# Performance work log

Hardware: AMD Instinct MI355X
Metric: run time of the kernel (lower is better)

## Reference

```python
import jax, jax.numpy as jnp
import numpy as np

B, S, DIM = 1, 2048, 4096
NH, NKV, HD = 32, 8, 128
REPEATS = NH // NKV
ROPE_THETA = 10000.0


def setup_inputs() -> dict:
    key = jax.random.key(0)
    ks = jax.random.split(key, 6)
    x = jax.random.normal(ks[0], (B, S, DIM), jnp.float32) * 0.02
    wq = jax.random.normal(ks[1], (NH * HD, DIM), jnp.float32) * 0.02
    wk = jax.random.normal(ks[2], (NKV * HD, DIM), jnp.float32) * 0.02
    wv = jax.random.normal(ks[3], (NKV * HD, DIM), jnp.float32) * 0.02
    wo = jax.random.normal(ks[4], (DIM, NH * HD), jnp.float32) * 0.02
    # rotary frequencies (real cos/sin form of complex freqs_cis)
    inv_freq = 1.0 / (ROPE_THETA ** (jnp.arange(0, HD, 2, dtype=jnp.float32) / HD))
    ang = jnp.arange(S, dtype=jnp.float32)[:, None] * inv_freq[None, :]  # [S, HD//2]
    freqs_cos = jnp.cos(ang)
    freqs_sin = jnp.sin(ang)
    positions = jnp.arange(S, dtype=jnp.int32)  # prompt phase: all positions
    # additive causal mask
    mask = jnp.where(jnp.tril(jnp.ones((S, S), bool)), 0.0, -1e9).astype(jnp.float32)
    cache_k = jnp.zeros((B, S, NKV, HD), jnp.float32)
    cache_v = jnp.zeros((B, S, NKV, HD), jnp.float32)
    return dict(x=x, wq=wq, wk=wk, wv=wv, wo=wo, freqs_cos=freqs_cos,
                freqs_sin=freqs_sin, cache_k=cache_k, cache_v=cache_v,
                positions=positions, mask=mask)


def apply_rope(t, cos, sin):
    # t: [b, s, h, d]; pairs are (d0,d1),(d2,d3),... matching view_as_complex
    tr = t[..., 0::2]
    ti = t[..., 1::2]
    c = cos[None, :, None, :]
    s = sin[None, :, None, :]
    out_r = tr * c - ti * s
    out_i = tr * s + ti * c
    return jnp.stack([out_r, out_i], axis=-1).reshape(t.shape)


def reference(x, wq, wk, wv, wo, freqs_cos, freqs_sin, cache_k, cache_v, positions, mask):
    b, s, _ = x.shape
    xq = jnp.einsum('bsd,od->bso', x, wq).reshape(b, s, NH, HD)
    xk = jnp.einsum('bsd,od->bso', x, wk).reshape(b, s, NKV, HD)
    xv = jnp.einsum('bsd,od->bso', x, wv).reshape(b, s, NKV, HD)
    xq = apply_rope(xq, freqs_cos, freqs_sin)
    xk = apply_rope(xk, freqs_cos, freqs_sin)
    # KV-cache scatter (prompt phase writes; output uses fresh xk/xv here)
    cache_k = cache_k.at[:, positions].set(xk)
    cache_v = cache_v.at[:, positions].set(xv)
    # GQA: repeat_interleave kv heads to match query heads
    k = jnp.repeat(xk, REPEATS, axis=2).transpose(0, 2, 1, 3)  # [b, NH, s, HD]
    v = jnp.repeat(xv, REPEATS, axis=2).transpose(0, 2, 1, 3)
    q = xq.transpose(0, 2, 1, 3)
    scale = HD ** -0.5
    scores = jnp.einsum('bhqd,bhkd->bhqk', q, k) * scale + mask[None, None]
    probs = jax.nn.softmax(scores.astype(jnp.float32), axis=-1).astype(q.dtype)
    out = jnp.einsum('bhqk,bhkd->bhqd', probs, v)
    out = out.transpose(0, 2, 1, 3).reshape(b, s, NH * HD)
    return jnp.einsum('bso,do->bsd', out, wo)
```

## Files before the change

### kernel.cpp

```cpp
#include <hip/hip_runtime.h>
#include <hip/hip_bf16.h>
#include <stdint.h>

typedef __bf16 bf16_t;
typedef __attribute__((ext_vector_type(8))) __bf16 bf16x8;
typedef __attribute__((ext_vector_type(4))) float f32x4;
typedef __attribute__((ext_vector_type(8))) unsigned short u16x8;

#define S_LEN 2048
#define DIM   4096
#define QKVN  6144
#define NHEAD 32
#define HDIM  128

typedef __attribute__((address_space(1))) unsigned int as1_u32;
typedef __attribute__((address_space(3))) unsigned int as3_u32;

__device__ __forceinline__ unsigned short f2bf(float f) {
  unsigned u = __builtin_bit_cast(unsigned, f);
  u += 0x7fffu + ((u >> 16) & 1u);
  return (unsigned short)(u >> 16);
}

__device__ __forceinline__ void gload_lds16(const void* g, void* l) {
  __builtin_amdgcn_global_load_lds(
      (as1_u32*)(unsigned long long)(uintptr_t)g,
      (as3_u32*)(unsigned int)(uintptr_t)l,
      16, 0, 0);
}

__global__ __launch_bounds__(256) void cvt5_kernel(const float* __restrict__ x,
                                                   const float* __restrict__ wq,
                                                   const float* __restrict__ wk,
                                                   const float* __restrict__ wv,
                                                   const float* __restrict__ wo,
                                                   ushort4* __restrict__ xb,
                                                   ushort4* __restrict__ wqkvb,
                                                   ushort4* __restrict__ wob) {
  const long N0 = 2097152;
  const long N1 = N0 + 4194304;
  const long N2 = N1 + 1048576;
  const long N3 = N2 + 1048576;
  const long N4 = N3 + 4194304;
  long idx = (long)blockIdx.x * 256 + threadIdx.x;
  long stride = (long)gridDim.x * 256;
  for (long i = idx; i < N4; i += stride) {
    const float4* s; ushort4* d; long o;
    if (i < N0)      { s = (const float4*)x;  d = xb;              o = i; }
    else if (i < N1) { s = (const float4*)wq; d = wqkvb;           o = i - N0; }
    else if (i < N2) { s = (const float4*)wk; d = wqkvb + 4194304; o = i - N1; }
    else if (i < N3) { s = (const float4*)wv; d = wqkvb + 5242880; o = i - N2; }
    else             { s = (const float4*)wo; d = wob;             o = i - N3; }
    float4 v = s[o];
    ushort4 r;
    r.x = f2bf(v.x); r.y = f2bf(v.y); r.z = f2bf(v.z); r.w = f2bf(v.w);
    d[o] = r;
  }
}

__device__ __forceinline__ bf16x8 fld(const char* half, int row, int chunk) {
  return *(const bf16x8*)(half + row * 128 + ((chunk ^ (row & 7)) << 4));
}

template <int OUTF32>
__global__ __launch_bounds__(512, 2) void gemm8q(const bf16_t* __restrict__ A,
                                                 const bf16_t* __restrict__ B,
                                                 void* __restrict__ Cout,
                                                 int M, int N, int K, int nxt) {
  __shared__ char lds[114688];
  const int tid = threadIdx.x;
  const int lane = tid & 63, w = tid >> 6;
  const int wm = w >> 2, wn = w & 3;
  const int lg = lane >> 4, lr = lane & 15;
  const int nwg = gridDim.x;
  const int orig = blockIdx.x;
  const int wgid = (orig & 7) * (nwg >> 3) + (orig >> 3);
  const int bx = wgid % nxt, by = wgid / nxt;
  const long rowA = (long)by * 256;
  const long rowB = (long)bx * 192;

  f32x4 acc[8][3];
  const f32x4 z4 = {0.f, 0.f, 0.f, 0.f};
#pragma unroll
  for (int i = 0; i < 8; ++i)
#pragma unroll
    for (int j = 0; j < 3; ++j) acc[i][j] = z4;

  const int r0 = tid >> 3, sl = tid & 7;
  const long xo  = (long)((sl ^ (r0 & 7)) << 3);
  const long aof = (rowA + r0) * (long)K + xo;
  const long bof = (rowB + r0) * (long)K + xo;
  const long j1  = (long)64 * K;
  const long h1  = (long)128 * K;
  const int ld0 = tid * 16, ld1 = (tid + 512) * 16, ld2 = (tid + 1024) * 16;

#define QSTG_A(K0, HALF, DBUF)                                                 \
  { char* hp = lds + (DBUF) * 57344 + (HALF) * 16384;                          \
    gload_lds16(A + aof + (HALF) * h1 + (K0),      hp + ld0);                  \
    gload_lds16(A + aof + (HALF) * h1 + j1 + (K0), hp + ld1); }
#define QSTG_B(K0, DBUF)                                                       \
  { char* bp = lds + (DBUF) * 57344 + 32768;                                   \
    gload_lds16(B + bof + (K0),          bp + ld0);                            \
    gload_lds16(B + bof + j1 + (K0),     bp + ld1);                            \
    gload_lds16(B + bof + 2 * j1 + (K0), bp + ld2); }

  const int nt = K >> 6;
  const int brow = wn * 48;

  QSTG_A(0, 0, 0); QSTG_A(0, 1, 0); QSTG_B(0, 0);
  QSTG_B(64, 1);
  asm volatile("s_waitcnt vmcnt(3)" ::: "memory");
  __builtin_amdgcn_s_barrier();

  bf16x8 af[8][2], bf_[3][2];

  for (int t = 0; t < nt; ++t) {
    const int d = t & 1;
    const char* Ah = lds + d * 57344 + wm * 16384;
    const char* Br = lds + d * 57344 + 32768;
    const int k1 = (t + 1) << 6, k2 = (t + 2) << 6;
#pragma unroll
    for (int m = 0; m < 2; ++m) {
      af[m][0] = fld(Ah, m * 16 + lr, lg);
      af[m][1] = fld(Ah, m * 16 + lr, 4 + lg);
    }
#pragma unroll
    for (int n = 0; n < 3; ++n) {
      bf_[n][0] = fld(Br, brow + n * 16 + lr, lg);
      bf_[n][1] = fld(Br, brow + n * 16 + lr, 4 + lg);
    }
    if (t + 1 < nt) QSTG_A(k1, 0, d ^ 1);
    __builtin_amdgcn_s_barrier();
    asm volatile("s_waitcnt lgkmcnt(0)" ::: "memory");
    __builtin_amdgcn_sched_barrier(0);
    __builtin_amdgcn_s_setprio(1);
#pragma unroll
    for (int m = 0; m < 2; ++m)
#pragma unroll
      for (int n = 0; n < 3; ++n) {
        acc[m][n] = __builtin_amdgcn_mfma_f32_16x16x32_bf16(af[m][0], bf_[n][0], acc[m][n], 0, 0, 0);
        acc[m][n] = __builtin_amdgcn_mfma_f32_16x16x32_bf16(af[m][1], bf_[n][1], acc[m][n], 0, 0, 0);
      }
    __builtin_amdgcn_s_setprio(0);
    __builtin_amdgcn_s_barrier();
#pragma unroll
    for (int m = 2; m < 4; ++m) {
      af[m][0] = fld(Ah, m * 16 + lr, lg);
      af[m][1] = fld(Ah, m * 16 + lr, 4 + lg);
    }
    if (t + 1 < nt) QSTG_A(k1, 1, d ^ 1);
    __builtin_amdgcn_s_barrier();
    asm volatile("s_waitcnt lgkmcnt(0)" ::: "memory");
    __builtin_amdgcn_sched_barrier(0);
    __builtin_amdgcn_s_setprio(1);
#pragma unroll
    for (int m = 2; m < 4; ++m)
#pragma unroll
      for (int n = 0; n < 3; ++n) {
        acc[m][n] = __builtin_amdgcn_mfma_f32_16x16x32_bf16(af[m][0], bf_[n][0], acc[m][n], 0, 0, 0);
        acc[m][n] = __builtin_amdgcn_mfma_f32_16x16x32_bf16(af[m][1], bf_[n][1], acc[m][n], 0, 0, 0);
      }
    __builtin_amdgcn_s_setprio(0);
    __builtin_amdgcn_s_barrier();
#pragma unroll
    for (int m = 4; m < 6; ++m) {
      af[m][0] = fld(Ah, m * 16 + lr, lg);
      af[m][1] = fld(Ah, m * 16 + lr, 4 + lg);
    }
    if (t + 2 < nt) QSTG_B(k2, d);
    __builtin_amdgcn_s_barrier();
    asm volatile("s_waitcnt lgkmcnt(0)" ::: "memory");
    __builtin_amdgcn_sched_barrier(0);
    __builtin_amdgcn_s_setprio(1);
#pragma unroll
    for (int m = 4; m < 6; ++m)
#pragma unroll
      for (int n = 0; n < 3; ++n) {
        acc[m][n] = __builtin_amdgcn_mfma_f32_16x16x32_bf16(af[m][0], bf_[n][0], acc[m][n], 0, 0, 0);
        acc[m][n] = __builtin_amdgcn_mfma_f32_16x16x32_bf16(af[m][1], bf_[n][1], acc[m][n], 0, 0, 0);
      }
    __builtin_amdgcn_s_setprio(0);
    __builtin_amdgcn_s_barrier();
#pragma unroll
    for (int m = 6; m < 8; ++m) {
      af[m][0] = fld(Ah, m * 16 + lr, lg);
      af[m][1] = fld(Ah, m * 16 + lr, 4 + lg);
    }
    __builtin_amdgcn_s_barrier();
    asm volatile("s_waitcnt lgkmcnt(0)" ::: "memory");
    __builtin_amdgcn_sched_barrier(0);
    __builtin_amdgcn_s_setprio(1);
#pragma unroll
    for (int m = 6; m < 8; ++m)
#pragma unroll
      for (int n = 0; n < 3; ++n) {
        acc[m][n] = __builtin_amdgcn_mfma_f32_16x16x32_bf16(af[m][0], bf_[n][0], acc[m][n], 0, 0, 0);
        acc[m][n] = __builtin_amdgcn_mfma_f32_16x16x32_bf16(af[m][1], bf_[n][1], acc[m][n], 0, 0, 0);
      }
    __builtin_amdgcn_s_setprio(0);
    if (t + 2 < nt) {
      asm volatile("s_waitcnt vmcnt(3)" ::: "memory");
    } else {
      asm volatile("s_waitcnt vmcnt(0)" ::: "memory");
    }
    __builtin_amdgcn_s_barrier();
  }
#undef QSTG_A
#undef QSTG_B

  const long crow = rowA + wm * 128;
  const long ccol = rowB + wn * 48;
  unsigned short* C = (unsigned short*)Cout;
#pragma unroll
  for (int mf = 0; mf < 8; ++mf)
#pragma unroll
    for (int j = 0; j < 4; ++j) {
      long row = crow + mf * 16 + lg * 4 + j;
      unsigned short* cp = C + row * N + ccol + lr;
#pragma unroll
      for (int nf = 0; nf < 3; ++nf) cp[nf * 16] = f2bf(acc[mf][nf][j]);
    }
}

template <int OUTF32>
__global__ __launch_bounds__(512, 2) void gemm2p(const bf16_t* __restrict__ A,
                                                 const bf16_t* __restrict__ B,
                                                 void* __restrict__ Cout,
                                                 int M, int N, int K, int nxt) {
  __shared__ char lds[147456];
  const int tid = threadIdx.x;
  const int lane = tid & 63, w = tid >> 6;
  const int wm = w >> 1, wn = w & 1;
  const int lg = lane >> 4, lr = lane & 15;
  const int nwg = gridDim.x;
  const int orig = blockIdx.x;
  const int wgid = (orig & 7) * (nwg >> 3) + (orig >> 3);
  const int bx = wgid % nxt, by = wgid / nxt;
  const long rowA = (long)by * 256;
  const long rowB = (long)bx * 128;

  f32x4 acc[4][4];
  const f32x4 z4 = {0.f, 0.f, 0.f, 0.f};
#pragma unroll
  for (int i = 0; i < 4; ++i)
#pragma unroll
    for (int j = 0; j < 4; ++j) acc[i][j] = z4;

  const int r0 = tid >> 3, sl = tid & 7;
  const long xo  = (long)((sl ^ (r0 & 7)) << 3);
  const long aof = (rowA + r0) * (long)K + xo;
  const long bof = (rowB + r0) * (long)K + xo;
  const long r64 = (long)64 * K;

#define PSTG_A(K0, BUF)                                                        \
  { char* ap = lds + (BUF) * 32768;                                            \
    gload_lds16(A + aof + (K0),           ap + tid * 16);                      \
    gload_lds16(A + aof + r64 + (K0),     ap + (tid + 512) * 16);              \
    gload_lds16(A + aof + 2 * r64 + (K0), ap + (tid + 1024) * 16);             \
    gload_lds16(A + aof + 3 * r64 + (K0), ap + (tid + 1536) * 16); }
#define PSTG_B(K0, BUF)                                                        \
  { char* bp = lds + 98304 + (BUF) * 16384;                                    \
    gload_lds16(B + bof + (K0),       bp + tid * 16);                          \
    gload_lds16(B + bof + r64 + (K0), bp + (tid + 512) * 16); }

  const int nt = K >> 6;

  PSTG_A(0, 0); PSTG_B(0, 0); PSTG_A(64, 1); PSTG_B(64, 1);
  asm volatile("s_waitcnt vmcnt(6)" ::: "memory");
  __builtin_amdgcn_s_barrier();

  bf16x8 af[4][2], bf_[4][2];

  for (int t = 0; t < nt; ++t) {
    const int b3 = t % 3, s3 = (t + 2) % 3;
    const char* Ab = lds + b3 * 32768;
    const char* Bb = lds + 98304 + b3 * 16384;
    const int arow = wm * 64, brow = wn * 64;
    const int k2 = (t + 2) << 6;
#pragma unroll
    for (int m = 0; m < 4; ++m) {
      af[m][0] = fld(Ab, arow + m * 16 + lr, lg);
      af[m][1] = fld(Ab, arow + m * 16 + lr, 4 + lg);
    }
#pragma unroll
    for (int n = 0; n < 2; ++n) {
      bf_[n][0] = fld(Bb, brow + n * 16 + lr, lg);
      bf_[n][1] = fld(Bb, brow + n * 16 + lr, 4 + lg);
    }
    if (t + 2 < nt) PSTG_A(k2, s3);
    __builtin_amdgcn_s_barrier();
    asm volatile("s_waitcnt lgkmcnt(0)" ::: "memory");
    __builtin_amdgcn_sched_barrier(0);
    __builtin_amdgcn_s_setprio(1);
#pragma unroll
    for (int m = 0; m < 4; ++m)
#pragma unroll
      for (int n = 0; n < 2; ++n) {
        acc[m][n] = __builtin_amdgcn_mfma_f32_16x16x32_bf16(af[m][0], bf_[n][0], acc[m][n], 0, 0, 0);
        acc[m][n] = __builtin_amdgcn_mfma_f32_16x16x32_bf16(af[m][1], bf_[n][1], acc[m][n], 0, 0, 0);
      }
    __builtin_amdgcn_s_setprio(0);
    __builtin_amdgcn_s_barrier();
#pragma unroll
    for (int n = 2; n < 4; ++n) {
      bf_[n][0] = fld(Bb, brow + n * 16 + lr, lg);
      bf_[n][1] = fld(Bb, brow + n * 16 + lr, 4 + lg);
    }
    if (t + 2 < nt) PSTG_B(k2, s3);
    __builtin_amdgcn_s_barrier();
    asm volatile("s_waitcnt lgkmcnt(0)" ::: "memory");
    __builtin_amdgcn_sched_barrier(0);
    __builtin_amdgcn_s_setprio(1);
#pragma unroll
    for (int m = 0; m < 4; ++m)
#pragma unroll
      for (int n = 2; n < 4; ++n) {
        acc[m][n] = __builtin_amdgcn_mfma_f32_16x16x32_bf16(af[m][0], bf_[n][0], acc[m][n], 0, 0, 0);
        acc[m][n] = __builtin_amdgcn_mfma_f32_16x16x32_bf16(af[m][1], bf_[n][1], acc[m][n], 0, 0, 0);
      }
    __builtin_amdgcn_s_setprio(0);
    if (t + 2 < nt) {
      asm volatile("s_waitcnt vmcnt(6)" ::: "memory");
    } else {
      asm volatile("s_waitcnt vmcnt(0)" ::: "memory");
    }
    __builtin_amdgcn_s_barrier();
  }
#undef PSTG_A
#undef PSTG_B

  const long crow = rowA + wm * 64;
  const long ccol = rowB + wn * 64;
  if (OUTF32) {
    float* C = (float*)Cout;
#pragma unroll
    for (int mf = 0; mf < 4; ++mf)
#pragma unroll
      for (int j = 0; j < 4; ++j) {
        long row = crow + mf * 16 + lg * 4 + j;
        float* cp = C + row * N + ccol + lr;
#pragma unroll
        for (int nf = 0; nf < 4; ++nf) cp[nf * 16] = acc[mf][nf][j];
      }
  } else {
    unsigned short* C = (unsigned short*)Cout;
#pragma unroll
    for (int mf = 0; mf < 4; ++mf)
#pragma unroll
      for (int j = 0; j < 4; ++j) {
        long row = crow + mf * 16 + lg * 4 + j;
        unsigned short* cp = C + row * N + ccol + lr;
#pragma unroll
        for (int nf = 0; nf < 4; ++nf) cp[nf * 16] = f2bf(acc[mf][nf][j]);
      }
  }
}

__global__ __launch_bounds__(256) void rope_kernel(unsigned int* __restrict__ qkv32,
                                                   const float* __restrict__ cosb,
                                                   const float* __restrict__ sinb) {
  int t = blockIdx.x * 256 + threadIdx.x;
  int i  = t & 63;
  int sh = t >> 6;
  int hh = sh % 40;
  int s  = sh / 40;
  int col2 = (hh < 32) ? (hh * 64 + i) : (2048 + (hh - 32) * 64 + i);
  unsigned int* p = qkv32 + (long)s * (QKVN / 2) + col2;
  unsigned int v = *p;
  float tr = __builtin_bit_cast(float, (v & 0xffffu) << 16);
  float ti = __builtin_bit_cast(float, v & 0xffff0000u);
  float c  = cosb[s * 64 + i];
  float sn = sinb[s * 64 + i];
  float orr = tr * c - ti * sn;
  float oi  = tr * sn + ti * c;
  *p = (unsigned int)f2bf(orr) | ((unsigned int)f2bf(oi) << 16);
}

__global__ __launch_bounds__(256) void vtrans_kernel(const bf16_t* __restrict__ qkv,
                                                     bf16_t* __restrict__ vT) {
  const int kh = blockIdx.x;
  const int hd = threadIdx.x & 127;
  const int s0 = blockIdx.y * 16 + (threadIdx.x >> 7) * 8;
  u16x8 v;
#pragma unroll
  for (int e = 0; e < 8; ++e)
    v[e] = *(const unsigned short*)(qkv + (long)(s0 + e) * QKVN + 5120 + kh * HDIM + hd);
  *(u16x8*)(vT + ((long)kh * HDIM + hd) * S_LEN + s0) = v;
}

__global__ __launch_bounds__(512) void attn_kernel(const bf16_t* __restrict__ qkv,
                                                   const bf16_t* __restrict__ vT,
                                                   unsigned short* __restrict__ ob) {
  __shared__ bf16_t Kt[64 * 128];
  __shared__ bf16_t Vt[128 * 64];
  __shared__ bf16_t Pl[8 * 16 * 64];
  const int h  = blockIdx.x;
  const int qi = 15 - (int)blockIdx.y;
  const int qb = qi * 128;
  const int kh = h >> 2;
  const int tid = threadIdx.x, lane = tid & 63, w = tid >> 6;
  const int lg = lane >> 4, lr = lane & 15;
  const int qrow0 = qb + w * 16;

  bf16x8 qf[4];
  const bf16_t* qptr = qkv + (long)(qrow0 + lr) * QKVN + h * HDIM + lg * 8;
#pragma unroll
  for (int kk = 0; kk < 4; ++kk) qf[kk] = *(const bf16x8*)(qptr + kk * 32);

  const f32x4 z4 = {0.f, 0.f, 0.f, 0.f};
  f32x4 oacc[8];
#pragma unroll
  for (int c = 0; c < 8; ++c) oacc[c] = z4;
  float m[4]    = {-1e30f, -1e30f, -1e30f, -1e30f};
  float lsum[4] = {0.f, 0.f, 0.f, 0.f};

  char* KtB = (char*)Kt;
  char* VtB = (char*)Vt;
  char* PlB = (char*)Pl + w * 2048;
  const float SCL2 = 0.08838834764831845f * 1.44269504088896f;
  const int ntiles = 2 * qi + 2;
  const int wqmax = qrow0 + 15;

  for (int t = 0; t < ntiles; ++t) {
    const int kv0 = t * 64;
    __syncthreads();
#pragma unroll
    for (int it = 0; it < 2; ++it) {
      int cch = tid + it * 512;
      int r = cch >> 4, c = cch & 15;
      const bf16_t* src = qkv + (long)(kv0 + r) * QKVN + 4096 + kh * HDIM
                          + ((c ^ (r & 7)) * 8);
      gload_lds16(src, KtB + cch * 16);
    }
#pragma unroll
    for (int it = 0; it < 2; ++it) {
      int cch = tid + it * 512;
      int hd = cch >> 3, c = cch & 7;
      const bf16_t* src = vT + ((long)kh * HDIM + hd) * S_LEN + kv0
                          + ((c ^ (hd & 7)) * 8);
      gload_lds16(src, VtB + cch * 16);
    }
    __syncthreads();
    if (kv0 > wqmax) continue;

    f32x4 sf[4];
#pragma unroll
    for (int f = 0; f < 4; ++f) {
      f32x4 a = z4;
      int n = f * 16 + lr;
      int rb = n * 256, sw = (n & 7) << 4;
#pragma unroll
      for (int kk = 0; kk < 4; ++kk) {
        bf16x8 kf = *(const bf16x8*)(KtB + rb + (((kk * 4 + lg) * 16) ^ sw));
        a = __builtin_amdgcn_mfma_f32_16x16x32_bf16(qf[kk], kf, a, 0, 0, 0);
      }
      sf[f] = a;
    }

    float sv[4][4], mx[4];
    if (kv0 + 63 <= qrow0) {
#pragma unroll
      for (int j = 0; j < 4; ++j) {
#pragma unroll
        for (int f = 0; f < 4; ++f) sv[j][f] = sf[f][j] * SCL2;
        float t0 = fmaxf(fmaxf(sv[j][0], sv[j][1]), fmaxf(sv[j][2], sv[j][3]));
        t0 = fmaxf(t0, __shfl_xor(t0, 1));
        t0 = fmaxf(t0, __shfl_xor(t0, 2));
        t0 = fmaxf(t0, __shfl_xor(t0, 4));
        t0 = fmaxf(t0, __shfl_xor(t0, 8));
        mx[j] = t0;
      }
    } else {
#pragma unroll
      for (int j = 0; j < 4; ++j) {
        int qrow = qrow0 + lg * 4 + j;
#pragma unroll
        for (int f = 0; f < 4; ++f) {
          float s = sf[f][j] * SCL2;
          if (kv0 + f * 16 + lr > qrow) s = -1e9f;
          sv[j][f] = s;
        }
        float t0 = fmaxf(fmaxf(sv[j][0], sv[j][1]), fmaxf(sv[j][2], sv[j][3]));
        t0 = fmaxf(t0, __shfl_xor(t0, 1));
        t0 = fmaxf(t0, __shfl_xor(t0, 2));
        t0 = fmaxf(t0, __shfl_xor(t0, 4));
        t0 = fmaxf(t0, __shfl_xor(t0, 8));
        mx[j] = t0;
      }
    }
    float g = fmaxf(fmaxf(mx[0] - m[0], mx[1] - m[1]),
                    fmaxf(mx[2] - m[2], mx[3] - m[3]));
    if (__any(g > 0.f)) {
#pragma unroll
      for (int j = 0; j < 4; ++j) {
        float mn = fmaxf(m[j], mx[j]);
        float sc;
        asm("v_exp_f32 %0, %1" : "=v"(sc) : "v"(m[j] - mn));
        lsum[j] *= sc;
        m[j] = mn;
#pragma unroll
        for (int c = 0; c < 8; ++c) oacc[c][j] *= sc;
      }
    }
#pragma unroll
    for (int j = 0; j < 4; ++j) {
      float p[4];
#pragma unroll
      for (int f = 0; f < 4; ++f)
        asm("v_exp_f32 %0, %1" : "=v"(p[f]) : "v"(sv[j][f] - m[j]));
      float ps = (p[0] + p[1]) + (p[2] + p[3]);
      ps += __shfl_xor(ps, 1);
      ps += __shfl_xor(ps, 2);
      ps += __shfl_xor(ps, 4);
      ps += __shfl_xor(ps, 8);
      lsum[j] += ps;
      int row = lg * 4 + j;
      int swp = (row & 7) << 4;
#pragma unroll
      for (int f = 0; f < 4; ++f)
        *(unsigned short*)(PlB + row * 128 + (((f * 16 + lr) * 2) ^ swp)) = f2bf(p[f]);
    }

    bf16x8 pfr[2];
#pragma unroll
    for (int kk = 0; kk < 2; ++kk)
      pfr[kk] = *(const bf16x8*)(PlB + lr * 128 + (((kk * 4 + lg) * 16) ^ ((lr & 7) << 4)));
#pragma unroll
    for (int c = 0; c < 8; ++c) {
      int hd = c * 16 + lr;
      int rb = hd * 128, sw = (hd & 7) << 4;
#pragma unroll
      for (int kk = 0; kk < 2; ++kk) {
        bf16x8 vf = *(const bf16x8*)(VtB + rb + (((kk * 4 + lg) * 16) ^ sw));
        oacc[c] = __builtin_amdgcn_mfma_f32_16x16x32_bf16(pfr[kk], vf, oacc[c], 0, 0, 0);
      }
    }
  }

  float rl[4];
#pragma unroll
  for (int j = 0; j < 4; ++j) rl[j] = 1.f / lsum[j];
#pragma unroll
  for (int c = 0; c < 8; ++c)
#pragma unroll
    for (int j = 0; j < 4; ++j) {
      long row = qrow0 + lg * 4 + j;
      ob[row * 4096 + h * 128 + c * 16 + lr] = f2bf(oacc[c][j] * rl[j]);
    }
}

extern "C" void kernel_launch(void* const* d_in, const int* in_sizes, int n_in,
                              void* d_out, int out_size, void* d_ws, size_t ws_size,
                              hipStream_t stream) {
  const float* x  = (const float*)d_in[0];
  const float* wq = (const float*)d_in[1];
  const float* wk = (const float*)d_in[2];
  const float* wv = (const float*)d_in[3];
  const float* wo = (const float*)d_in[4];
  const float* fc = (const float*)d_in[5];
  const float* fs = (const float*)d_in[6];

  char* ws = (char*)d_ws;
  bf16_t* xb    = (bf16_t*)(ws + 0);
  bf16_t* wqkvb = (bf16_t*)(ws + 16777216);
  bf16_t* wob   = (bf16_t*)(ws + 67108864);
  bf16_t* qkv   = (bf16_t*)(ws + 100663296);
  bf16_t* ob    = (bf16_t*)(ws + 125829120);
  bf16_t* vT    = (bf16_t*)(ws + 0);

  cvt5_kernel<<<2048, 256, 0, stream>>>(x, wq, wk, wv, wo,
                                        (ushort4*)xb, (ushort4*)wqkvb, (ushort4*)wob);

  gemm8q<0><<<256, 512, 0, stream>>>(xb, wqkvb, qkv, 2048, 6144, 4096, 32);
  vtrans_kernel<<<dim3(8, 128), 256, 0, stream>>>(qkv, vT);
  rope_kernel<<<20480, 256, 0, stream>>>((unsigned int*)qkv, fc, fs);
  attn_kernel<<<dim3(32, 16), 512, 0, stream>>>(qkv, vT, (unsigned short*)ob);
  gemm2p<1><<<256, 512, 0, stream>>>(ob, wob, d_out, 2048, 4096, 4096, 32);
}
```

Before: 320.9 us.

## Deepen GEMM A-tile prefetch to triple buffer and double-buffer attention KV loads

The GEMM kernel now keeps three A-tile stages in LDS (148 KB total) and prefetches A two K-steps ahead, with the vmcnt waits adjusted to match. The attention kernel gets double-buffered K/V LDS tiles, so the loads for tile t+2 are issued while tile t is being computed, replacing the load-then-sync pattern on every iteration. The goal is to hide global-memory latency behind MFMA work. The cost is more LDS per block, which can lower occupancy: the GEMM asks for 2 blocks per CU with 148 KB each, and that may no longer fit.

```diff
diff --git a/kernel.cpp b/kernel.cpp
--- a/kernel.cpp
+++ b/kernel.cpp
@@ -67,7 +67,7 @@
                                                  const bf16_t* __restrict__ B,
                                                  void* __restrict__ Cout,
                                                  int M, int N, int K, int nxt) {
-  __shared__ char lds[114688];
+  __shared__ char lds[147456];
   const int tid = threadIdx.x;
   const int lane = tid & 63, w = tid >> 6;
   const int wm = w >> 2, wn = w & 3;
@@ -94,12 +94,12 @@
   const long h1  = (long)128 * K;
   const int ld0 = tid * 16, ld1 = (tid + 512) * 16, ld2 = (tid + 1024) * 16;
 
-#define QSTG_A(K0, HALF, DBUF)                                                 \
-  { char* hp = lds + (DBUF) * 57344 + (HALF) * 16384;                          \
+#define QSTG_A(K0, HALF, BUF3)                                                 \
+  { char* hp = lds + (BUF3) * 32768 + (HALF) * 16384;                          \
     gload_lds16(A + aof + (HALF) * h1 + (K0),      hp + ld0);                  \
     gload_lds16(A + aof + (HALF) * h1 + j1 + (K0), hp + ld1); }
 #define QSTG_B(K0, DBUF)                                                       \
-  { char* bp = lds + (DBUF) * 57344 + 32768;                                   \
+  { char* bp = lds + 98304 + (DBUF) * 24576;                                   \
     gload_lds16(B + bof + (K0),          bp + ld0);                            \
     gload_lds16(B + bof + j1 + (K0),     bp + ld1);                            \
     gload_lds16(B + bof + 2 * j1 + (K0), bp + ld2); }
@@ -108,17 +108,17 @@
   const int brow = wn * 48;
 
   QSTG_A(0, 0, 0); QSTG_A(0, 1, 0); QSTG_B(0, 0);
-  QSTG_B(64, 1);
-  asm volatile("s_waitcnt vmcnt(3)" ::: "memory");
+  QSTG_A(64, 0, 1); QSTG_A(64, 1, 1); QSTG_B(64, 1);
+  asm volatile("s_waitcnt vmcnt(7)" ::: "memory");
   __builtin_amdgcn_s_barrier();
 
   bf16x8 af[8][2], bf_[3][2];
 
   for (int t = 0; t < nt; ++t) {
-    const int d = t & 1;
-    const char* Ah = lds + d * 57344 + wm * 16384;
-    const char* Br = lds + d * 57344 + 32768;
-    const int k1 = (t + 1) << 6, k2 = (t + 2) << 6;
+    const int a3 = t % 3, s3 = (t + 2) % 3, d = t & 1;
+    const char* Ah = lds + a3 * 32768 + wm * 16384;
+    const char* Br = lds + 98304 + d * 24576;
+    const int k2 = (t + 2) << 6;
 #pragma unroll
     for (int m = 0; m < 2; ++m) {
       af[m][0] = fld(Ah, m * 16 + lr, lg);
@@ -129,7 +129,7 @@
       bf_[n][0] = fld(Br, brow + n * 16 + lr, lg);
       bf_[n][1] = fld(Br, brow + n * 16 + lr, 4 + lg);
     }
-    if (t + 1 < nt) QSTG_A(k1, 0, d ^ 1);
+    if (t + 2 < nt) QSTG_A(k2, 0, s3);
     __builtin_amdgcn_s_barrier();
     asm volatile("s_waitcnt lgkmcnt(0)" ::: "memory");
     __builtin_amdgcn_sched_barrier(0);
@@ -148,7 +148,7 @@
       af[m][0] = fld(Ah, m * 16 + lr, lg);
       af[m][1] = fld(Ah, m * 16 + lr, 4 + lg);
     }
-    if (t + 1 < nt) QSTG_A(k1, 1, d ^ 1);
+    if (t + 2 < nt) QSTG_A(k2, 1, s3);
     __builtin_amdgcn_s_barrier();
     asm volatile("s_waitcnt lgkmcnt(0)" ::: "memory");
     __builtin_amdgcn_sched_barrier(0);
@@ -199,7 +199,7 @@
       }
     __builtin_amdgcn_s_setprio(0);
     if (t + 2 < nt) {
-      asm volatile("s_waitcnt vmcnt(3)" ::: "memory");
+      asm volatile("s_waitcnt vmcnt(7)" ::: "memory");
     } else {
       asm volatile("s_waitcnt vmcnt(0)" ::: "memory");
     }
@@ -391,8 +391,8 @@
 __global__ __launch_bounds__(512) void attn_kernel(const bf16_t* __restrict__ qkv,
                                                    const bf16_t* __restrict__ vT,
                                                    unsigned short* __restrict__ ob) {
-  __shared__ bf16_t Kt[64 * 128];
-  __shared__ bf16_t Vt[128 * 64];
+  __shared__ bf16_t Kt[2][64 * 128];
+  __shared__ bf16_t Vt[2][128 * 64];
   __shared__ bf16_t Pl[8 * 16 * 64];
   const int h  = blockIdx.x;
   const int qi = 15 - (int)blockIdx.y;
@@ -414,128 +414,147 @@
   float m[4]    = {-1e30f, -1e30f, -1e30f, -1e30f};
   float lsum[4] = {0.f, 0.f, 0.f, 0.f};
 
-  char* KtB = (char*)Kt;
-  char* VtB = (char*)Vt;
   char* PlB = (char*)Pl + w * 2048;
   const float SCL2 = 0.08838834764831845f * 1.44269504088896f;
   const int ntiles = 2 * qi + 2;
   const int wqmax = qrow0 + 15;
 
+#define STAGE_KV(T, BUF)                                                       \
+  {                                                                            \
+    const int kvs = (T) * 64;                                                  \
+    _Pragma("unroll")                                                          \
+    for (int it = 0; it < 2; ++it) {                                           \
+      int cch = tid + it * 512;                                                \
+      int r = cch >> 4, c = cch & 15;                                          \
+      gload_lds16(qkv + (long)(kvs + r) * QKVN + 4096 + kh * HDIM              \
+                      + ((c ^ (r & 7)) * 8),                                   \
+                  (char*)Kt[BUF] + cch * 16);                                  \
+    }                                                                          \
+    _Pragma("unroll")                                                          \
+    for (int it = 0; it < 2; ++it) {                                           \
+      int cch = tid + it * 512;                                                \
+      int hd2 = cch >> 3, c = cch & 7;                                         \
+      gload_lds16(vT + ((long)kh * HDIM + hd2) * S_LEN + kvs                   \
+                      + ((c ^ (hd2 & 7)) * 8),                                 \
+                  (char*)Vt[BUF] + cch * 16);                                  \
+    }                                                                          \
+  }
+
+  STAGE_KV(0, 0);
+  STAGE_KV(1, 1);
+  asm volatile("s_waitcnt vmcnt(4)" ::: "memory");
+  __builtin_amdgcn_s_barrier();
+
   for (int t = 0; t < ntiles; ++t) {
     const int kv0 = t * 64;
-    __syncthreads();
-#pragma unroll
-    for (int it = 0; it < 2; ++it) {
-      int cch = tid + it * 512;
-      int r = cch >> 4, c = cch & 15;
-      const bf16_t* src = qkv + (long)(kv0 + r) * QKVN + 4096 + kh * HDIM
-                          + ((c ^ (r & 7)) * 8);
-      gload_lds16(src, KtB + cch * 16);
-    }
-#pragma unroll
-    for (int it = 0; it < 2; ++it) {
-      int cch = tid + it * 512;
-      int hd = cch >> 3, c = cch & 7;
-      const bf16_t* src = vT + ((long)kh * HDIM + hd) * S_LEN + kv0
-                          + ((c ^ (hd & 7)) * 8);
-      gload_lds16(src, VtB + cch * 16);
-    }
-    __syncthreads();
-    if (kv0 > wqmax) continue;
-
-    f32x4 sf[4];
-#pragma unroll
-    for (int f = 0; f < 4; ++f) {
-      f32x4 a = z4;
-      int n = f * 16 + lr;
-      int rb = n * 256, sw = (n & 7) << 4;
-#pragma unroll
-      for (int kk = 0; kk < 4; ++kk) {
-        bf16x8 kf = *(const bf16x8*)(KtB + rb + (((kk * 4 + lg) * 16) ^ sw));
-        a = __builtin_amdgcn_mfma_f32_16x16x32_bf16(qf[kk], kf, a, 0, 0, 0);
-      }
-      sf[f] = a;
-    }
-
-    float sv[4][4], mx[4];
-    if (kv0 + 63 <= qrow0) {
+    const int d = t & 1;
+    if (kv0 <= wqmax) {
+      char* KtB = (char*)Kt[d];
+      char* VtB = (char*)Vt[d];
+
+      f32x4 sf[4];
+#pragma unroll
+      for (int f = 0; f < 4; ++f) {
+        f32x4 a = z4;
+        int n = f * 16 + lr;
+        int rb = n * 256, sw = (n & 7) << 4;
+#pragma unroll
+        for (int kk = 0; kk < 4; ++kk) {
+          bf16x8 kf = *(const bf16x8*)(KtB + rb + (((kk * 4 + lg) * 16) ^ sw));
+          a = __builtin_amdgcn_mfma_f32_16x16x32_bf16(qf[kk], kf, a, 0, 0, 0);
+        }
+        sf[f] = a;
+      }
+
+      float sv[4][4], mx[4];
+      if (kv0 + 63 <= qrow0) {
+#pragma unroll
+        for (int j = 0; j < 4; ++j) {
+#pragma unroll
+          for (int f = 0; f < 4; ++f) sv[j][f] = sf[f][j] * SCL2;
+          float t0 = fmaxf(fmaxf(sv[j][0], sv[j][1]), fmaxf(sv[j][2], sv[j][3]));
+          t0 = fmaxf(t0, __shfl_xor(t0, 1));
+          t0 = fmaxf(t0, __shfl_xor(t0, 2));
+          t0 = fmaxf(t0, __shfl_xor(t0, 4));
+          t0 = fmaxf(t0, __shfl_xor(t0, 8));
+          mx[j] = t0;
+        }
+      } else {
+#pragma unroll
+        for (int j = 0; j < 4; ++j) {
+          int qrow = qrow0 + lg * 4 + j;
+#pragma unroll
+          for (int f = 0; f < 4; ++f) {
+            float s = sf[f][j] * SCL2;
+            if (kv0 + f * 16 + lr > qrow) s = -1e9f;
+            sv[j][f] = s;
+          }
+          float t0 = fmaxf(fmaxf(sv[j][0], sv[j][1]), fmaxf(sv[j][2], sv[j][3]));
+          t0 = fmaxf(t0, __shfl_xor(t0, 1));
+          t0 = fmaxf(t0, __shfl_xor(t0, 2));
+          t0 = fmaxf(t0, __shfl_xor(t0, 4));
+          t0 = fmaxf(t0, __shfl_xor(t0, 8));
+          mx[j] = t0;
+        }
+      }
+      float g = fmaxf(fmaxf(mx[0] - m[0], mx[1] - m[1]),
+                      fmaxf(mx[2] - m[2], mx[3] - m[3]));
+      if (__any(g > 0.f)) {
+#pragma unroll
+        for (int j = 0; j < 4; ++j) {
+          float mn = fmaxf(m[j], mx[j]);
+          float sc;
+          asm("v_exp_f32 %0, %1" : "=v"(sc) : "v"(m[j] - mn));
+          lsum[j] *= sc;
+          m[j] = mn;
+#pragma unroll
+          for (int c = 0; c < 8; ++c) oacc[c][j] *= sc;
+        }
+      }
 #pragma unroll
       for (int j = 0; j < 4; ++j) {
-#pragma unroll
-        for (int f = 0; f < 4; ++f) sv[j][f] = sf[f][j] * SCL2;
-        float t0 = fmaxf(fmaxf(sv[j][0], sv[j][1]), fmaxf(sv[j][2], sv[j][3]));
-        t0 = fmaxf(t0, __shfl_xor(t0, 1));
-        t0 = fmaxf(t0, __shfl_xor(t0, 2));
-        t0 = fmaxf(t0, __shfl_xor(t0, 4));
-        t0 = fmaxf(t0, __shfl_xor(t0, 8));
-        mx[j] = t0;
-      }
+        float p[4];
+#pragma unroll
+        for (int f = 0; f < 4; ++f)
+          asm("v_exp_f32 %0, %1" : "=v"(p[f]) : "v"(sv[j][f] - m[j]));
+        float ps = (p[0] + p[1]) + (p[2] + p[3]);
+        ps += __shfl_xor(ps, 1);
+        ps += __shfl_xor(ps, 2);
+        ps += __shfl_xor(ps, 4);
+        ps += __shfl_xor(ps, 8);
+        lsum[j] += ps;
+        int row = lg * 4 + j;
+        int swp = (row & 7) << 4;
+#pragma unroll
+        for (int f = 0; f < 4; ++f)
+          *(unsigned short*)(PlB + row * 128 + (((f * 16 + lr) * 2) ^ swp)) = f2bf(p[f]);
+      }
+
+      bf16x8 pfr[2];
+#pragma unroll
+      for (int kk = 0; kk < 2; ++kk)
+        pfr[kk] = *(const bf16x8*)(PlB + lr * 128 + (((kk * 4 + lg) * 16) ^ ((lr & 7) << 4)));
+#pragma unroll
+      for (int c = 0; c < 8; ++c) {
+        int hd = c * 16 + lr;
+        int rb = hd * 128, sw = (hd & 7) << 4;
+#pragma unroll
+        for (int kk = 0; kk < 2; ++kk) {
+          bf16x8 vf = *(const bf16x8*)(VtB + rb + (((kk * 4 + lg) * 16) ^ sw));
+          oacc[c] = __builtin_amdgcn_mfma_f32_16x16x32_bf16(pfr[kk], vf, oacc[c], 0, 0, 0);
+        }
+      }
+    }
+    __builtin_amdgcn_s_barrier();
+    if (t + 2 < ntiles) {
+      STAGE_KV(t + 2, d);
+      asm volatile("s_waitcnt vmcnt(4)" ::: "memory");
     } else {
-#pragma unroll
-      for (int j = 0; j < 4; ++j) {
-        int qrow = qrow0 + lg * 4 + j;
-#pragma unroll
-        for (int f = 0; f < 4; ++f) {
-          float s = sf[f][j] * SCL2;
-          if (kv0 + f * 16 + lr > qrow) s = -1e9f;
-          sv[j][f] = s;
-        }
-        float t0 = fmaxf(fmaxf(sv[j][0], sv[j][1]), fmaxf(sv[j][2], sv[j][3]));
-        t0 = fmaxf(t0, __shfl_xor(t0, 1));
-        t0 = fmaxf(t0, __shfl_xor(t0, 2));
-        t0 = fmaxf(t0, __shfl_xor(t0, 4));
-        t0 = fmaxf(t0, __shfl_xor(t0, 8));
-        mx[j] = t0;
-      }
-    }
-    float g = fmaxf(fmaxf(mx[0] - m[0], mx[1] - m[1]),
-                    fmaxf(mx[2] - m[2], mx[3] - m[3]));
-    if (__any(g > 0.f)) {
-#pragma unroll
-      for (int j = 0; j < 4; ++j) {
-        float mn = fmaxf(m[j], mx[j]);
-        float sc;
-        asm("v_exp_f32 %0, %1" : "=v"(sc) : "v"(m[j] - mn));
-        lsum[j] *= sc;
-        m[j] = mn;
-#pragma unroll
-        for (int c = 0; c < 8; ++c) oacc[c][j] *= sc;
-      }
-    }
-#pragma unroll
-    for (int j = 0; j < 4; ++j) {
-      float p[4];
-#pragma unroll
-      for (int f = 0; f < 4; ++f)
-        asm("v_exp_f32 %0, %1" : "=v"(p[f]) : "v"(sv[j][f] - m[j]));
-      float ps = (p[0] + p[1]) + (p[2] + p[3]);
-      ps += __shfl_xor(ps, 1);
-      ps += __shfl_xor(ps, 2);
-      ps += __shfl_xor(ps, 4);
-      ps += __shfl_xor(ps, 8);
-      lsum[j] += ps;
-      int row = lg * 4 + j;
-      int swp = (row & 7) << 4;
-#pragma unroll
-      for (int f = 0; f < 4; ++f)
-        *(unsigned short*)(PlB + row * 128 + (((f * 16 + lr) * 2) ^ swp)) = f2bf(p[f]);
-    }
-
-    bf16x8 pfr[2];
-#pragma unroll
-    for (int kk = 0; kk < 2; ++kk)
-      pfr[kk] = *(const bf16x8*)(PlB + lr * 128 + (((kk * 4 + lg) * 16) ^ ((lr & 7) << 4)));
-#pragma unroll
-    for (int c = 0; c < 8; ++c) {
-      int hd = c * 16 + lr;
-      int rb = hd * 128, sw = (hd & 7) << 4;
-#pragma unroll
-      for (int kk = 0; kk < 2; ++kk) {
-        bf16x8 vf = *(const bf16x8*)(VtB + rb + (((kk * 4 + lg) * 16) ^ sw));
-        oacc[c] = __builtin_amdgcn_mfma_f32_16x16x32_bf16(pfr[kk], vf, oacc[c], 0, 0, 0);
-      }
-    }
+      asm volatile("s_waitcnt vmcnt(0)" ::: "memory");
+    }
+    __builtin_amdgcn_s_barrier();
   }
+#undef STAGE_KV
 
   float rl[4];
 #pragma unroll
```

Result: no change. 320.1 us (-0.3%).
